# Performance work log

Hardware: AMD Instinct MI355X
Metric: run time of the kernel (lower is better)

## Reference

```python
import jax, jax.numpy as jnp
import numpy as np

N_NODES = 1_000_000
N_EDGES = 32_000_000
EPS_INIT = 100.0


def setup_inputs() -> dict:
    key = jax.random.key(0)
    ks = jax.random.split(key, 8)
    x = jax.random.normal(ks[0], (N_NODES, 1), dtype=jnp.float32)
    edge_index = jax.random.randint(ks[1], (2, N_EDGES), 0, N_NODES, dtype=jnp.int64)
    # MLP params: Linear(1,20) -> ReLU -> Linear(20,20) -> ReLU -> Linear(20,1)
    w1 = jax.random.normal(ks[2], (1, 20), dtype=jnp.float32) / np.sqrt(1.0)
    b1 = jnp.zeros((20,), dtype=jnp.float32)
    w2 = jax.random.normal(ks[3], (20, 20), dtype=jnp.float32) / np.sqrt(20.0)
    b2 = jnp.zeros((20,), dtype=jnp.float32)
    w3 = jax.random.normal(ks[4], (20, 1), dtype=jnp.float32) / np.sqrt(20.0)
    b3 = jnp.zeros((1,), dtype=jnp.float32)
    eps = jnp.asarray(EPS_INIT, dtype=jnp.float32)
    return {"x": x, "edge_index": edge_index, "eps": eps,
            "w1": w1, "b1": b1, "w2": w2, "b2": b2, "w3": w3, "b3": b3}


def reference(x, edge_index, eps, w1, b1, w2, b2, w3, b3):
    # GINConv: out = MLP((1 + eps) * x + sum_{j in N(i)} x_j)
    src, dst = edge_index[0], edge_index[1]
    # gather source features per edge, scatter-add to destination nodes
    agg = jax.ops.segment_sum(x[src], dst, num_segments=N_NODES)  # [N, 1]
    h = (1.0 + eps) * x + agg
    h = jax.nn.relu(h @ w1 + b1)   # [N, 20]
    h = jax.nn.relu(h @ w2 + b2)   # [N, 20]
    out = h @ w3 + b3              # [N, 1]
    return out
```

## Files before the change

kernel.cpp:

```cpp
#include <hip/hip_runtime.h>

#define N_NODES 1000000
#define N_EDGES 32000000

#define NB        256
#define TSC       1024
#define EPB       125000
#define QPB       31250
#define NBKT      245
#define BKT_PAD   256
#define CAP       135168
#define RING      96
#define RSTRIDE   97

#define BINS_ELEMS  ((size_t)NBKT * CAP)
#define CNT_ELEMS   ((size_t)NB * BKT_PAD)
#define PAGG_ELEMS  ((size_t)NBKT * 2 * 4096)
#define WS_NEEDED   ((BINS_ELEMS + CNT_ELEMS + BKT_PAD + PAGG_ELEMS) * 4)


__global__ __launch_bounds__(TSC) void gin_count(const int* __restrict__ dst,
                                                 unsigned* __restrict__ cnt) {
    __shared__ unsigned h[BKT_PAD];
    int tid = threadIdx.x;
    if (tid < BKT_PAD) h[tid] = 0u;
    __syncthreads();
    int k = blockIdx.x;
    const int4* q = reinterpret_cast<const int4*>(dst) + (size_t)k * QPB;
    for (int base = 0; base < QPB; base += TSC * 4) {
        int i0 = base + tid, i1 = i0 + TSC, i2 = i1 + TSC, i3 = i2 + TSC;
        int4 d0 = {0,0,0,0}, d1 = {0,0,0,0}, d2 = {0,0,0,0}, d3 = {0,0,0,0};
        bool v0 = i0 < QPB, v1 = i1 < QPB, v2 = i2 < QPB, v3 = i3 < QPB;
        if (v0) d0 = q[i0];
        if (v1) d1 = q[i1];
        if (v2) d2 = q[i2];
        if (v3) d3 = q[i3];
        if (v0) { atomicAdd(&h[d0.x >> 12], 1u); atomicAdd(&h[d0.y >> 12], 1u);
                  atomicAdd(&h[d0.z >> 12], 1u); atomicAdd(&h[d0.w >> 12], 1u); }
        if (v1) { atomicAdd(&h[d1.x >> 12], 1u); atomicAdd(&h[d1.y >> 12], 1u);
                  atomicAdd(&h[d1.z >> 12], 1u); atomicAdd(&h[d1.w >> 12], 1u); }
        if (v2) { atomicAdd(&h[d2.x >> 12], 1u); atomicAdd(&h[d2.y >> 12], 1u);
                  atomicAdd(&h[d2.z >> 12], 1u); atomicAdd(&h[d2.w >> 12], 1u); }
        if (v3) { atomicAdd(&h[d3.x >> 12], 1u); atomicAdd(&h[d3.y >> 12], 1u);
                  atomicAdd(&h[d3.z >> 12], 1u); atomicAdd(&h[d3.w >> 12], 1u); }
    }
    __syncthreads();
    if (tid < BKT_PAD) cnt[(size_t)k * BKT_PAD + tid] = h[tid];
}

__global__ void gin_scan(unsigned* __restrict__ cnt, unsigned* __restrict__ tot) {
    int gtid = blockIdx.x * blockDim.x + threadIdx.x;
    int b = gtid >> 6;
    int lane = gtid & 63;
    if (b >= BKT_PAD) return;
    unsigned running = 0;
    for (int base = 0; base < NB; base += 64) {
        int idx = base + lane;
        unsigned v = (idx < NB) ? cnt[(size_t)idx * BKT_PAD + b] : 0u;
        unsigned s = v;
        for (int d = 1; d < 64; d <<= 1) {
            unsigned u = __shfl_up(s, d);
            if (lane >= d) s += u;
        }
        unsigned excl = s - v;
        if (idx < NB) cnt[(size_t)idx * BKT_PAD + b] = running + excl;
        running += __shfl(s, 63);
    }
    if (lane == 0) tot[b] = running;
}

__global__ __launch_bounds__(TSC) void gin_scatter_bins(const int* __restrict__ src,
                                                        const int* __restrict__ dst,
                                                        const unsigned* __restrict__ cnt,
                                                        unsigned* __restrict__ bins) {
    __shared__ unsigned stage[BKT_PAD][RSTRIDE];
    __shared__ unsigned stot[BKT_PAD];
    __shared__ unsigned sflt[BKT_PAD];
    __shared__ unsigned sbase[BKT_PAD];

    int tid = threadIdx.x;
    int k = blockIdx.x;
    if (tid < BKT_PAD) {
        stot[tid] = 0u;
        sflt[tid] = 0u;
        sbase[tid] = cnt[(size_t)k * BKT_PAD + tid];
    }
    __syncthreads();

    const int4* qs = reinterpret_cast<const int4*>(src) + (size_t)k * QPB;
    const int4* qd = reinterpret_cast<const int4*>(dst) + (size_t)k * QPB;

    int4 s_cur = {0,0,0,0}, d_cur = {0,0,0,0};
    bool v_cur = tid < QPB;
    if (v_cur) { s_cur = qs[tid]; d_cur = qd[tid]; }

    for (int t0 = 0; t0 < QPB; t0 += TSC) {
        int nx = t0 + TSC + tid;
        int4 s_nxt = {0,0,0,0}, d_nxt = {0,0,0,0};
        bool v_nxt = nx < QPB;
        if (v_nxt) { s_nxt = qs[nx]; d_nxt = qd[nx]; }

        if (v_cur) {
#define PUT(ss, dd) do {                                                     \
            unsigned b_ = (unsigned)(dd) >> 12;                              \
            unsigned p_ = atomicAdd(&stot[b_], 1u);                          \
            stage[b_][p_ % RING] =                                           \
                (((unsigned)(dd) & 4095u) << 20) | (unsigned)(ss);           \
        } while (0)
            PUT(s_cur.x, d_cur.x);
            PUT(s_cur.y, d_cur.y);
            PUT(s_cur.z, d_cur.z);
            PUT(s_cur.w, d_cur.w);
#undef PUT
        }
        __syncthreads();
        if (tid < BKT_PAD) {
            unsigned b = (unsigned)tid;
            unsigned T = stot[b];
            unsigned F = sflt[b];
            if (F + 32 <= T) {
                unsigned gbase = sbase[b];
                unsigned* gout = bins + (size_t)b * CAP;
                while (F + 32 <= T) {
                    unsigned r = F % RING;
                    unsigned gp = gbase + F;
                    if (gp + 32 <= CAP) {
#pragma unroll
                        for (int c = 0; c < 32; ++c) gout[gp + c] = stage[b][r + c];
                    }
                    F += 32;
                }
                sflt[b] = F;
            }
        }
        __syncthreads();
        s_cur = s_nxt; d_cur = d_nxt; v_cur = v_nxt;
    }
    if (tid < BKT_PAD) {
        unsigned b = (unsigned)tid;
        unsigned T = stot[b];
        unsigned F = sflt[b];
        unsigned gbase = sbase[b];
        unsigned* gout = bins + (size_t)b * CAP;
        for (; F < T; ++F) {
            unsigned gp = gbase + F;
            if (gp < CAP) gout[gp] = stage[b][F % RING];
        }
    }
}

__global__ __launch_bounds__(1024) void gin_reduce(const unsigned* __restrict__ bins,
                                                   const unsigned* __restrict__ tot,
                                                   const float* __restrict__ x,
                                                   float* __restrict__ pagg) {
    __shared__ float acc[4096];
    int tid = threadIdx.x;
    int blk = blockIdx.x;
    int b = blk >> 1;
    int h = blk & 1;
    for (int i = tid; i < 4096; i += 1024) acc[i] = 0.0f;
    __syncthreads();

    unsigned n = tot[b];
    if (n > CAP) n = CAP;
    const unsigned* bb = bins + (size_t)b * CAP;
    const uint4* bb4 = reinterpret_cast<const uint4*>(bb);
    unsigned nq = n >> 2;
    unsigned q_lo = h ? (nq >> 1) : 0;
    unsigned q_hi = h ? nq : (nq >> 1);

    unsigned i = q_lo + tid;
    for (; i + 3072 < q_hi; i += 4096) {
        uint4 e0 = bb4[i];
        uint4 e1 = bb4[i + 1024];
        uint4 e2 = bb4[i + 2048];
        uint4 e3 = bb4[i + 3072];
        float v0x = x[e0.x & 0xFFFFFu], v0y = x[e0.y & 0xFFFFFu];
        float v0z = x[e0.z & 0xFFFFFu], v0w = x[e0.w & 0xFFFFFu];
        float v1x = x[e1.x & 0xFFFFFu], v1y = x[e1.y & 0xFFFFFu];
        float v1z = x[e1.z & 0xFFFFFu], v1w = x[e1.w & 0xFFFFFu];
        float v2x = x[e2.x & 0xFFFFFu], v2y = x[e2.y & 0xFFFFFu];
        float v2z = x[e2.z & 0xFFFFFu], v2w = x[e2.w & 0xFFFFFu];
        float v3x = x[e3.x & 0xFFFFFu], v3y = x[e3.y & 0xFFFFFu];
        float v3z = x[e3.z & 0xFFFFFu], v3w = x[e3.w & 0xFFFFFu];
        atomicAdd(&acc[e0.x >> 20], v0x); atomicAdd(&acc[e0.y >> 20], v0y);
        atomicAdd(&acc[e0.z >> 20], v0z); atomicAdd(&acc[e0.w >> 20], v0w);
        atomicAdd(&acc[e1.x >> 20], v1x); atomicAdd(&acc[e1.y >> 20], v1y);
        atomicAdd(&acc[e1.z >> 20], v1z); atomicAdd(&acc[e1.w >> 20], v1w);
        atomicAdd(&acc[e2.x >> 20], v2x); atomicAdd(&acc[e2.y >> 20], v2y);
        atomicAdd(&acc[e2.z >> 20], v2z); atomicAdd(&acc[e2.w >> 20], v2w);
        atomicAdd(&acc[e3.x >> 20], v3x); atomicAdd(&acc[e3.y >> 20], v3y);
        atomicAdd(&acc[e3.z >> 20], v3z); atomicAdd(&acc[e3.w >> 20], v3w);
    }
    for (; i < q_hi; i += 1024) {
        uint4 e = bb4[i];
        atomicAdd(&acc[e.x >> 20], x[e.x & 0xFFFFFu]);
        atomicAdd(&acc[e.y >> 20], x[e.y & 0xFFFFFu]);
        atomicAdd(&acc[e.z >> 20], x[e.z & 0xFFFFFu]);
        atomicAdd(&acc[e.w >> 20], x[e.w & 0xFFFFFu]);
    }
    if (h) {
        for (unsigned j = (nq << 2) + tid; j < n; j += 1024) {
            unsigned e = bb[j];
            atomicAdd(&acc[e >> 20], x[e & 0xFFFFFu]);
        }
    }
    __syncthreads();

    float* po = pagg + (size_t)blk * 4096;
    for (int j = tid; j < 4096; j += 1024) po[j] = acc[j];
}

__global__ __launch_bounds__(512) void gin_combine_mlp(const float* __restrict__ pagg,
                               const float* __restrict__ x,
                               const float* __restrict__ eps,
                               const float* __restrict__ w1,
                               const float* __restrict__ b1,
                               const float* __restrict__ w2,
                               const float* __restrict__ b2,
                               const float* __restrict__ w3,
                               const float* __restrict__ b3,
                               float* __restrict__ out) {
    int i = blockIdx.x * blockDim.x + threadIdx.x;
    if (i >= N_NODES) return;
    int b = i >> 12;
    int j = i & 4095;
    float agg = pagg[(size_t)(b * 2) * 4096 + j] + pagg[(size_t)(b * 2 + 1) * 4096 + j];
    float h0 = (1.0f + eps[0]) * x[i] + agg;

    float h1[20];
#pragma unroll
    for (int jj = 0; jj < 20; ++jj)
        h1[jj] = fmaxf(fmaf(h0, w1[jj], b1[jj]), 0.0f);

    float o = b3[0];
#pragma unroll
    for (int kk = 0; kk < 20; ++kk) {
        float a = b2[kk];
#pragma unroll
        for (int jj = 0; jj < 20; ++jj)
            a = fmaf(h1[jj], w2[jj * 20 + kk], a);
        o = fmaf(fmaxf(a, 0.0f), w3[kk], o);
    }
    out[i] = o;
}

__global__ void gin_zero_kernel(float* __restrict__ agg, int n) {
    int i = blockIdx.x * blockDim.x + threadIdx.x;
    if (i < n) agg[i] = 0.0f;
}

__global__ void gin_scatter_kernel(const float* __restrict__ x,
                                   const int* __restrict__ src,
                                   const int* __restrict__ dst,
                                   float* __restrict__ agg) {
    int q = blockIdx.x * blockDim.x + threadIdx.x;
    int e = q * 4;
    if (e + 3 < N_EDGES) {
        int4 s = *reinterpret_cast<const int4*>(src + e);
        int4 d = *reinterpret_cast<const int4*>(dst + e);
        atomicAdd(&agg[d.x], x[s.x]);
        atomicAdd(&agg[d.y], x[s.y]);
        atomicAdd(&agg[d.z], x[s.z]);
        atomicAdd(&agg[d.w], x[s.w]);
    } else if (e < N_EDGES) {
        for (; e < N_EDGES; ++e) atomicAdd(&agg[dst[e]], x[src[e]]);
    }
}

__global__ void gin_mlp_kernel(const float* __restrict__ x,
                               const float* __restrict__ agg,
                               const float* __restrict__ eps,
                               const float* __restrict__ w1,
                               const float* __restrict__ b1,
                               const float* __restrict__ w2,
                               const float* __restrict__ b2,
                               const float* __restrict__ w3,
                               const float* __restrict__ b3,
                               float* __restrict__ out) {
    int i = blockIdx.x * blockDim.x + threadIdx.x;
    if (i >= N_NODES) return;
    float h0 = (1.0f + eps[0]) * x[i] + agg[i];
    float h1[20];
#pragma unroll
    for (int j = 0; j < 20; ++j) h1[j] = fmaxf(fmaf(h0, w1[j], b1[j]), 0.0f);
    float o = b3[0];
#pragma unroll
    for (int k = 0; k < 20; ++k) {
        float a = b2[k];
#pragma unroll
        for (int j = 0; j < 20; ++j) a = fmaf(h1[j], w2[j * 20 + k], a);
        o = fmaf(fmaxf(a, 0.0f), w3[k], o);
    }
    out[i] = o;
}

extern "C" void kernel_launch(void* const* d_in, const int* in_sizes, int n_in,
                              void* d_out, int out_size, void* d_ws, size_t ws_size,
                              hipStream_t stream) {
    const float* x    = (const float*)d_in[0];
    const int*   ei   = (const int*)  d_in[1];
    const float* eps  = (const float*)d_in[2];
    const float* w1   = (const float*)d_in[3];
    const float* b1   = (const float*)d_in[4];
    const float* w2   = (const float*)d_in[5];
    const float* b2   = (const float*)d_in[6];
    const float* w3   = (const float*)d_in[7];
    const float* b3   = (const float*)d_in[8];
    float* out = (float*)d_out;

    const int* src = ei;
    const int* dst = ei + N_EDGES;

    if (ws_size >= WS_NEEDED) {
        unsigned* bins = (unsigned*)d_ws;
        unsigned* cnt  = bins + BINS_ELEMS;
        unsigned* tot  = cnt + CNT_ELEMS;
        float*    pagg = (float*)(tot + BKT_PAD);

        gin_count<<<NB, TSC, 0, stream>>>(dst, cnt);
        {
            int blocks = (BKT_PAD * 64 + 255) / 256;
            gin_scan<<<blocks, 256, 0, stream>>>(cnt, tot);
        }
        gin_scatter_bins<<<NB, TSC, 0, stream>>>(src, dst, cnt, bins);
        gin_reduce<<<NBKT * 2, 1024, 0, stream>>>(bins, tot, x, pagg);
        gin_combine_mlp<<<(N_NODES + 511) / 512, 512, 0, stream>>>(pagg, x, eps,
                                                 w1, b1, w2, b2, w3, b3, out);
    } else {
        float* agg = (ws_size >= (size_t)N_NODES * sizeof(float)) ? (float*)d_ws : out;
        {
            int blocks = (N_NODES + 255) / 256;
            gin_zero_kernel<<<blocks, 256, 0, stream>>>(agg, N_NODES);
        }
        {
            int quads = N_EDGES / 4;
            int blocks = (quads + 255) / 256;
            gin_scatter_kernel<<<blocks, 256, 0, stream>>>(x, src, dst, agg);
        }
        {
            int blocks = (N_NODES + 255) / 256;
            gin_mlp_kernel<<<blocks, 256, 0, stream>>>(x, agg, eps, w1, b1, w2, b2,
                                                       w3, b3, out);
        }
    }
}
```

Baseline: 407.0 us.

## Use nontemporal streaming loads and a work queue to parallelize bin flushes

Replaces plain vector loads of src/dst and bin entries with nontemporal loads so streamed data is less likely to evict the reused x array from cache. The flush phase of the scatter kernel changes from one thread per bucket writing 32 elements serially to a shared queue of 32-element chunks, each written by 32 lanes in parallel for coalesced stores. The reduce kernel drops its 4-way unrolled loop in favor of a simple loop, which lowers memory-level parallelism per thread. The queue adds an extra barrier and shared-memory bookkeeping per iteration.

```diff
diff --git a/kernel.cpp b/kernel.cpp
--- a/kernel.cpp
+++ b/kernel.cpp
@@ -12,11 +12,15 @@
 #define CAP       135168
 #define RING      96
 #define RSTRIDE   97
+#define QSIZE     1024
 
 #define BINS_ELEMS  ((size_t)NBKT * CAP)
 #define CNT_ELEMS   ((size_t)NB * BKT_PAD)
 #define PAGG_ELEMS  ((size_t)NBKT * 2 * 4096)
 #define WS_NEEDED   ((BINS_ELEMS + CNT_ELEMS + BKT_PAD + PAGG_ELEMS) * 4)
+
+typedef int  iv4 __attribute__((ext_vector_type(4)));
+typedef unsigned uv4 __attribute__((ext_vector_type(4)));
 
 
 __global__ __launch_bounds__(TSC) void gin_count(const int* __restrict__ dst,
@@ -26,15 +30,15 @@
     if (tid < BKT_PAD) h[tid] = 0u;
     __syncthreads();
     int k = blockIdx.x;
-    const int4* q = reinterpret_cast<const int4*>(dst) + (size_t)k * QPB;
+    const iv4* q = reinterpret_cast<const iv4*>(dst) + (size_t)k * QPB;
     for (int base = 0; base < QPB; base += TSC * 4) {
         int i0 = base + tid, i1 = i0 + TSC, i2 = i1 + TSC, i3 = i2 + TSC;
-        int4 d0 = {0,0,0,0}, d1 = {0,0,0,0}, d2 = {0,0,0,0}, d3 = {0,0,0,0};
+        iv4 d0 = {0,0,0,0}, d1 = {0,0,0,0}, d2 = {0,0,0,0}, d3 = {0,0,0,0};
         bool v0 = i0 < QPB, v1 = i1 < QPB, v2 = i2 < QPB, v3 = i3 < QPB;
-        if (v0) d0 = q[i0];
-        if (v1) d1 = q[i1];
-        if (v2) d2 = q[i2];
-        if (v3) d3 = q[i3];
+        if (v0) d0 = __builtin_nontemporal_load(&q[i0]);
+        if (v1) d1 = __builtin_nontemporal_load(&q[i1]);
+        if (v2) d2 = __builtin_nontemporal_load(&q[i2]);
+        if (v3) d3 = __builtin_nontemporal_load(&q[i3]);
         if (v0) { atomicAdd(&h[d0.x >> 12], 1u); atomicAdd(&h[d0.y >> 12], 1u);
                   atomicAdd(&h[d0.z >> 12], 1u); atomicAdd(&h[d0.w >> 12], 1u); }
         if (v1) { atomicAdd(&h[d1.x >> 12], 1u); atomicAdd(&h[d1.y >> 12], 1u);
@@ -77,6 +81,8 @@
     __shared__ unsigned stot[BKT_PAD];
     __shared__ unsigned sflt[BKT_PAD];
     __shared__ unsigned sbase[BKT_PAD];
+    __shared__ unsigned queue[QSIZE];
+    __shared__ unsigned qcount;
 
     int tid = threadIdx.x;
     int k = blockIdx.x;
@@ -85,21 +91,29 @@
         sflt[tid] = 0u;
         sbase[tid] = cnt[(size_t)k * BKT_PAD + tid];
     }
-    __syncthreads();
-
-    const int4* qs = reinterpret_cast<const int4*>(src) + (size_t)k * QPB;
-    const int4* qd = reinterpret_cast<const int4*>(dst) + (size_t)k * QPB;
-
-    int4 s_cur = {0,0,0,0}, d_cur = {0,0,0,0};
+    if (tid == 0) qcount = 0;
+    __syncthreads();
+
+    const iv4* qs = reinterpret_cast<const iv4*>(src) + (size_t)k * QPB;
+    const iv4* qd = reinterpret_cast<const iv4*>(dst) + (size_t)k * QPB;
+
+    iv4 s_cur = {0,0,0,0}, d_cur = {0,0,0,0};
     bool v_cur = tid < QPB;
-    if (v_cur) { s_cur = qs[tid]; d_cur = qd[tid]; }
+    if (v_cur) {
+        s_cur = __builtin_nontemporal_load(&qs[tid]);
+        d_cur = __builtin_nontemporal_load(&qd[tid]);
+    }
 
     for (int t0 = 0; t0 < QPB; t0 += TSC) {
         int nx = t0 + TSC + tid;
-        int4 s_nxt = {0,0,0,0}, d_nxt = {0,0,0,0};
+        iv4 s_nxt = {0,0,0,0}, d_nxt = {0,0,0,0};
         bool v_nxt = nx < QPB;
-        if (v_nxt) { s_nxt = qs[nx]; d_nxt = qd[nx]; }
-
+        if (v_nxt) {
+            s_nxt = __builtin_nontemporal_load(&qs[nx]);
+            d_nxt = __builtin_nontemporal_load(&qd[nx]);
+        }
+
+        if (tid == 0) qcount = 0;
         if (v_cur) {
 #define PUT(ss, dd) do {                                                     \
             unsigned b_ = (unsigned)(dd) >> 12;                              \
@@ -115,27 +129,34 @@
         }
         __syncthreads();
         if (tid < BKT_PAD) {
-            unsigned b = (unsigned)tid;
-            unsigned T = stot[b];
-            unsigned F = sflt[b];
-            if (F + 32 <= T) {
-                unsigned gbase = sbase[b];
-                unsigned* gout = bins + (size_t)b * CAP;
-                while (F + 32 <= T) {
-                    unsigned r = F % RING;
-                    unsigned gp = gbase + F;
-                    if (gp + 32 <= CAP) {
-#pragma unroll
-                        for (int c = 0; c < 32; ++c) gout[gp + c] = stage[b][r + c];
-                    }
-                    F += 32;
-                }
-                sflt[b] = F;
+            unsigned T = stot[tid], F = sflt[tid];
+            unsigned nch = (T - F) >> 5;
+            if (nch) {
+                unsigned off = atomicAdd(&qcount, nch);
+                for (unsigned c = 0; c < nch; ++c)
+                    queue[off + c] = ((unsigned)tid << 3) | c;
             }
         }
         __syncthreads();
+        {
+            unsigned C = qcount;
+            unsigned lane = tid & 31;
+            for (unsigned g = tid >> 5; g < C; g += TSC / 32) {
+                unsigned qe = queue[g];
+                unsigned b = qe >> 3, c = qe & 7;
+                unsigned pos = sflt[b] + (c << 5) + lane;
+                unsigned gp = sbase[b] + pos;
+                if (gp < CAP) bins[(size_t)b * CAP + gp] = stage[b][pos % RING];
+            }
+        }
+        __syncthreads();
+        if (tid < BKT_PAD) {
+            unsigned T = stot[tid], F = sflt[tid];
+            sflt[tid] = F + (((T - F) >> 5) << 5);
+        }
         s_cur = s_nxt; d_cur = d_nxt; v_cur = v_nxt;
     }
+    __syncthreads();
     if (tid < BKT_PAD) {
         unsigned b = (unsigned)tid;
         unsigned T = stot[b];
@@ -164,36 +185,12 @@
     unsigned n = tot[b];
     if (n > CAP) n = CAP;
     const unsigned* bb = bins + (size_t)b * CAP;
-    const uint4* bb4 = reinterpret_cast<const uint4*>(bb);
+    const uv4* bb4 = reinterpret_cast<const uv4*>(bb);
     unsigned nq = n >> 2;
     unsigned q_lo = h ? (nq >> 1) : 0;
     unsigned q_hi = h ? nq : (nq >> 1);
-
-    unsigned i = q_lo + tid;
-    for (; i + 3072 < q_hi; i += 4096) {
-        uint4 e0 = bb4[i];
-        uint4 e1 = bb4[i + 1024];
-        uint4 e2 = bb4[i + 2048];
-        uint4 e3 = bb4[i + 3072];
-        float v0x = x[e0.x & 0xFFFFFu], v0y = x[e0.y & 0xFFFFFu];
-        float v0z = x[e0.z & 0xFFFFFu], v0w = x[e0.w & 0xFFFFFu];
-        float v1x = x[e1.x & 0xFFFFFu], v1y = x[e1.y & 0xFFFFFu];
-        float v1z = x[e1.z & 0xFFFFFu], v1w = x[e1.w & 0xFFFFFu];
-        float v2x = x[e2.x & 0xFFFFFu], v2y = x[e2.y & 0xFFFFFu];
-        float v2z = x[e2.z & 0xFFFFFu], v2w = x[e2.w & 0xFFFFFu];
-        float v3x = x[e3.x & 0xFFFFFu], v3y = x[e3.y & 0xFFFFFu];
-        float v3z = x[e3.z & 0xFFFFFu], v3w = x[e3.w & 0xFFFFFu];
-        atomicAdd(&acc[e0.x >> 20], v0x); atomicAdd(&acc[e0.y >> 20], v0y);
-        atomicAdd(&acc[e0.z >> 20], v0z); atomicAdd(&acc[e0.w >> 20], v0w);
-        atomicAdd(&acc[e1.x >> 20], v1x); atomicAdd(&acc[e1.y >> 20], v1y);
-        atomicAdd(&acc[e1.z >> 20], v1z); atomicAdd(&acc[e1.w >> 20], v1w);
-        atomicAdd(&acc[e2.x >> 20], v2x); atomicAdd(&acc[e2.y >> 20], v2y);
-        atomicAdd(&acc[e2.z >> 20], v2z); atomicAdd(&acc[e2.w >> 20], v2w);
-        atomicAdd(&acc[e3.x >> 20], v3x); atomicAdd(&acc[e3.y >> 20], v3y);
-        atomicAdd(&acc[e3.z >> 20], v3z); atomicAdd(&acc[e3.w >> 20], v3w);
-    }
-    for (; i < q_hi; i += 1024) {
-        uint4 e = bb4[i];
+    for (unsigned i = q_lo + tid; i < q_hi; i += 1024) {
+        uv4 e = __builtin_nontemporal_load(&bb4[i]);
         atomicAdd(&acc[e.x >> 20], x[e.x & 0xFFFFFu]);
         atomicAdd(&acc[e.y >> 20], x[e.y & 0xFFFFFu]);
         atomicAdd(&acc[e.z >> 20], x[e.z & 0xFFFFFu]);
@@ -201,7 +198,7 @@
     }
     if (h) {
         for (unsigned j = (nq << 2) + tid; j < n; j += 1024) {
-            unsigned e = bb[j];
+            unsigned e = __builtin_nontemporal_load(&bb[j]);
             atomicAdd(&acc[e >> 20], x[e & 0xFFFFFu]);
         }
     }
```

Result: faster. 364.6 us (-10.4%).
